# Kernel tuning notes

Measured on AMD Instinct MI355X. Metric: run time of the kernel, lower is better.

Reference implementation:

```python
import math
import jax, jax.numpy as jnp
import numpy as np

DRAGON_ITERATIONS = 12
DRAGON_SMOOTHING = 0.1


def _dragon_patterns(iterations=DRAGON_ITERATIONS, smoothing=DRAGON_SMOOTHING):
    """Deterministic (non-learned) Dragon curve patterns, matching torch impl."""
    patterns = [np.array([0.5], dtype=np.float32)]
    kernel = np.ones(3, dtype=np.float32) / 3.0
    for _ in range(1, iterations):
        prev = patterns[-1]
        n = len(prev)
        newp = np.zeros(2 * n + 1, dtype=np.float32)
        newp[:n] = prev
        newp[n] = 0.5
        newp[n + 1:] = 1.0 - prev[::-1]
        if smoothing > 0:
            # conv1d with kernel_size=3, padding=1 (zero pad) == np.convolve 'same'
            newp = np.convolve(newp, kernel, mode='same').astype(np.float32)
        newp = (newp - newp.min()) / (newp.max() - newp.min() + 1e-8)
        patterns.append(newp.astype(np.float32))
    return patterns

_PATTERNS = _dragon_patterns()


def _interp_pattern(seq_len):
    """Linearly interpolate selected dragon pattern to seq_len (static shapes)."""
    it = min(int(math.log2(seq_len)), DRAGON_ITERATIONS - 1)
    pattern = _PATTERNS[it]
    if len(pattern) == seq_len:
        w = pattern.copy()
    else:
        x_old = np.linspace(0.0, 1.0, len(pattern), dtype=np.float64)
        x_new = np.linspace(0.0, 1.0, seq_len, dtype=np.float64)
        w = np.interp(x_new, x_old, pattern.astype(np.float64)).astype(np.float32)
    return it, jnp.asarray(w)


def setup_inputs() -> dict:
    key = jax.random.key(0)
    ks = jax.random.split(key, 8)
    B, S, D = 8, 2048, 512
    query = jax.random.normal(ks[0], (B, S, D), dtype=jnp.float32)
    k = jax.random.normal(ks[1], (B, S, D), dtype=jnp.float32)
    value = jax.random.normal(ks[2], (B, S, D), dtype=jnp.float32)
    pattern_scale = jnp.ones((DRAGON_ITERATIONS,), dtype=jnp.float32)
    pattern_bias = jnp.zeros((DRAGON_ITERATIONS,), dtype=jnp.float32)
    w1 = jax.random.normal(ks[3], (DRAGON_ITERATIONS, 64), dtype=jnp.float32) * (1.0 / math.sqrt(DRAGON_ITERATIONS))
    b1 = jnp.zeros((64,), dtype=jnp.float32)
    w2 = jax.random.normal(ks[4], (64, 1), dtype=jnp.float32) * (1.0 / 8.0)
    b2 = jnp.zeros((1,), dtype=jnp.float32)
    return {"query": query, "key": k, "value": value,
            "pattern_scale": pattern_scale, "pattern_bias": pattern_bias,
            "w1": w1, "b1": b1, "w2": w2, "b2": b2}


def reference(query, key, value, pattern_scale, pattern_bias, w1, b1, w2, b2):
    B, S, D = key.shape
    it, base_w = _interp_pattern(S)
    # learned affine + softplus on dragon weights
    dragon_w = jax.nn.softplus(base_w * pattern_scale[it] + pattern_bias[it])  # [S]
    weighted_keys = key * dragon_w[None, :, None]                              # [B,S,D]
    scores = jnp.einsum('bqd,bkd->bqk', query, weighted_keys) / math.sqrt(D)   # [B,S,S]
    attn = jax.nn.softmax(scores, axis=-1)
    # blend factor from one-hot iteration features through tiny MLP
    feat = jax.nn.one_hot(it, DRAGON_ITERATIONS, dtype=query.dtype)            # [12]
    h = jax.nn.relu(feat @ w1 + b1)
    blend = jax.nn.sigmoid(h @ w2 + b2)                                        # [1]
    blend = blend[0]
    final_attn = blend * attn + (1.0 - blend) / S                              # uniform blend
    out = jnp.einsum('bqk,bkd->bqd', final_attn, value)                        # [B,S,D]
    # original does output.squeeze(1); S>1 so it's a no-op here
    return out
```

## Files before the change

### kernel.cpp

```cpp
#include <hip/hip_runtime.h>
#include <cstdint>

#define DEV __device__ __forceinline__

typedef float f32x4 __attribute__((ext_vector_type(4)));
typedef short s16x8 __attribute__((ext_vector_type(8)));

DEV unsigned short f2bf(float f){
    unsigned u = __builtin_bit_cast(unsigned, f);
    u = u + 0x7fffu + ((u >> 16) & 1u);
    return (unsigned short)(u >> 16);
}
DEV float bf2f(unsigned short h){
    unsigned u = ((unsigned)h) << 16;
    return __builtin_bit_cast(float, u);
}

typedef const void __attribute__((address_space(1)))* gcp;
typedef void __attribute__((address_space(3)))* lp;
DEV void gload_lds16(const void* g, void* l){
    __builtin_amdgcn_global_load_lds((gcp)g, (lp)l, 16, 0, 0);
}

#define SCALE_QK 0.04419417382415922f

struct Pat2 { float v[2048]; };
constexpr Pat2 make_pat2(){
    float a[4095] = {}; float b[4095] = {};
    a[0] = 0.5f; int len = 1;
    for (int it = 1; it < 12; ++it){
        int n = len, nl = 2*n + 1;
        for (int i = 0; i < nl; ++i)
            b[i] = (i < n) ? a[i] : ((i == n) ? 0.5f : 1.0f - a[2*n - i]);
        const float third = 1.0f/3.0f;
        float mn = 3.4e38f, mx = -3.4e38f;
        for (int i = 0; i < nl; ++i){
            float s = b[i]*third;
            if (i > 0)      s += b[i-1]*third;
            if (i < nl - 1) s += b[i+1]*third;
            a[i] = s;
            mn = (s < mn) ? s : mn;
            mx = (s > mx) ? s : mx;
        }
        float d = mx - mn + 1e-8f;
        for (int i = 0; i < nl; ++i) a[i] = (a[i] - mn) / d;
        len = nl;
    }
    Pat2 p{};
    for (int i = 0; i < 2048; ++i) p.v[i] = a[2*i];
    return p;
}
__device__ const Pat2 g_pat2 = make_pat2();

__global__ __launch_bounds__(256) void k_conv(
    const float* __restrict__ Q, const float* __restrict__ K,
    const float* __restrict__ V,
    unsigned short* __restrict__ Qb, unsigned short* __restrict__ Kb,
    unsigned short* __restrict__ Vt, float* __restrict__ vmean)
{
    __shared__ float sh[4480];
    int tid = threadIdx.x;
    int bx  = blockIdx.x;

    if (bx < 1024){
        const long long total4 = (long long)8*2048*512/4;
        long long stride = 1024LL*256;
        for (long long i = (long long)bx*256 + tid; i < total4; i += stride){
            long long base = i*4;
            const float4 q = *(const float4*)(Q + base);
            const float4 k = *(const float4*)(K + base);
            ushort4 qo, ko;
            qo.x = f2bf(q.x); qo.y = f2bf(q.y); qo.z = f2bf(q.z); qo.w = f2bf(q.w);
            ko.x = f2bf(k.x); ko.y = f2bf(k.y); ko.z = f2bf(k.z); ko.w = f2bf(k.w);
            *(ushort4*)(Qb + base) = qo;
            *(ushort4*)(Kb + base) = ko;
        }
        return;
    }

    int t = bx - 1024;
    int stile = t & 31, dtile = (t >> 5) & 7, b = t >> 8;
    int s0 = stile*64, d0 = dtile*64;
    float (*tile)[66] = (float(*)[66])sh;
    float* red = sh + 4224;
    int tx = tid & 63, ty = tid >> 6;
    const float* src = V + ((long long)b*2048 + s0)*512 + d0;
    #pragma unroll
    for (int r = 0; r < 16; ++r){
        int row = r*4 + ty;
        tile[row][tx] = src[(long long)row*512 + tx];
    }
    __syncthreads();
    unsigned short* dst = Vt + ((long long)b*512 + d0)*2048 + s0;
    #pragma unroll
    for (int r = 0; r < 16; ++r){
        int drow = r*4 + ty;
        dst[(long long)drow*2048 + tx] = f2bf(tile[tx][drow]);
    }
    int dcol = tid & 63, sp = tid >> 6;
    float s = 0.f;
    #pragma unroll
    for (int ii = 0; ii < 16; ++ii) s += tile[sp*16 + ii][dcol];
    red[sp*64 + dcol] = s;
    __syncthreads();
    if (sp == 0){
        float tot = red[dcol] + red[64+dcol] + red[128+dcol] + red[192+dcol];
        atomicAdd(&vmean[b*512 + d0 + dcol], tot * (1.0f/2048.0f));
    }
}

#define EPAD 140

__global__ __launch_bounds__(256) void k_gemm_qk(
    const unsigned short* __restrict__ Qb, const unsigned short* __restrict__ Kb,
    const float* __restrict__ scale, const float* __restrict__ bias,
    unsigned short* __restrict__ Sp)
{
    __shared__ unsigned short smem[128*EPAD];
    unsigned short* At = smem;
    unsigned short* Bt = smem + 8192;
    int tid = threadIdx.x;
    int lane = tid & 63, wave = tid >> 6;
    int wm = wave >> 1, wn = wave & 1;
    int ln = lane & 15, q4 = lane >> 4;
    int sx = ln & 7;
    int q0 = blockIdx.y*128, k0 = blockIdx.x*128, b = blockIdx.z;
    const unsigned short* Abase = Qb + ((long long)b*2048 + q0)*512;
    const unsigned short* Bbase = Kb + ((long long)b*2048 + k0)*512;

    f32x4 acc[4][4];
    #pragma unroll
    for (int i = 0; i < 4; ++i)
        #pragma unroll
        for (int j = 0; j < 4; ++j) acc[i][j] = (f32x4)0.0f;

    int cc = lane & 7, rg = lane >> 3;
    for (int kt = 0; kt < 8; ++kt){
        #pragma unroll
        for (int c = 0; c < 4; ++c){
            int chunk = wave*4 + c;
            int row = chunk*8 + rg;
            int gc  = cc ^ (row & 7);
            gload_lds16(Abase + (long long)row*512 + kt*64 + gc*8, &At[chunk*512]);
            gload_lds16(Bbase + (long long)row*512 + kt*64 + gc*8, &Bt[chunk*512]);
        }
        __syncthreads();
        #pragma unroll
        for (int ks = 0; ks < 2; ++ks){
            int cs = ((ks*4 + q4) ^ sx) * 8;
            s16x8 af[4], bfr[4];
            #pragma unroll
            for (int i = 0; i < 4; ++i)
                af[i] = *(const s16x8*)&At[(wm*64 + i*16 + ln)*64 + cs];
            #pragma unroll
            for (int j = 0; j < 4; ++j)
                bfr[j] = *(const s16x8*)&Bt[(wn*64 + j*16 + ln)*64 + cs];
            #pragma unroll
            for (int i = 0; i < 4; ++i)
                #pragma unroll
                for (int j = 0; j < 4; ++j)
                    acc[i][j] = __builtin_amdgcn_mfma_f32_16x16x32_bf16(af[i], bfr[j], acc[i][j], 0, 0, 0);
        }
        __syncthreads();
    }

    float sc = scale[11], bi = bias[11];
    float wq[4];
    #pragma unroll
    for (int j = 0; j < 4; ++j){
        float x = g_pat2.v[k0 + wn*64 + j*16 + ln]*sc + bi;
        wq[j] = (fmaxf(x, 0.f) + log1pf(__expf(-fabsf(x)))) * SCALE_QK;
    }
    #pragma unroll
    for (int i = 0; i < 4; ++i)
        #pragma unroll
        for (int j = 0; j < 4; ++j)
            #pragma unroll
            for (int r = 0; r < 4; ++r){
                int ql = wm*64 + i*16 + q4*4 + r;
                int kl = wn*64 + j*16 + ln;
                smem[ql*EPAD + kl] = f2bf(__expf(acc[i][j][r] * wq[j]));
            }
    __syncthreads();
    int row = tid >> 1, half = tid & 1;
    unsigned short* dstp = Sp + (long long)b*2048*2048
                              + (long long)(q0 + row)*2048 + k0 + half*64;
    const unsigned short* srcp = &smem[row*EPAD + half*64];
    #pragma unroll
    for (int u = 0; u < 8; ++u)
        *(s16x8*)(dstp + u*8) = *(const s16x8*)(srcp + u*8);
}

__global__ __launch_bounds__(256) void k_gemm_pv(
    const unsigned short* __restrict__ Sp, const unsigned short* __restrict__ Vt,
    const float* __restrict__ vmean,
    const float* __restrict__ w1, const float* __restrict__ b1,
    const float* __restrict__ w2, const float* __restrict__ b2,
    float* __restrict__ out)
{
    __shared__ unsigned short At[128*64];
    __shared__ unsigned short Bt[128*64];
    __shared__ float l_sh[128];
    __shared__ float sh_blend;
    int tid = threadIdx.x;
    int lane = tid & 63, wave = tid >> 6;
    int wm = wave >> 1, wn = wave & 1;
    int ln = lane & 15, q4 = lane >> 4;
    int sx = ln & 7;

    if (wave == 0){
        float h = fmaxf(w1[11*64 + lane] + b1[lane], 0.f);
        float c = h * w2[lane];
        #pragma unroll
        for (int off = 32; off > 0; off >>= 1) c += __shfl_xor(c, off, 64);
        if (lane == 0) sh_blend = 1.f/(1.f + __expf(-(c + b2[0])));
    }

    int g    = blockIdx.x;
    int xcd  = g & 7, slot = g >> 3;
    int pair = xcd*16 + (slot >> 2);
    int dt   = slot & 3;
    int qt   = pair & 15, b = pair >> 4;
    int q0 = qt*128, d0 = dt*128;

    const unsigned short* Abase = Sp + (long long)b*2048*2048 + (long long)q0*2048;
    const unsigned short* Bbase = Vt + ((long long)b*512 + d0)*2048;

    f32x4 acc[4][4];
    #pragma unroll
    for (int i = 0; i < 4; ++i)
        #pragma unroll
        for (int j = 0; j < 4; ++j) acc[i][j] = (f32x4)0.0f;
    float lsum[4] = {0.f, 0.f, 0.f, 0.f};

    int cc = lane & 7, rg = lane >> 3;
    for (int kt = 0; kt < 32; ++kt){
        #pragma unroll
        for (int c = 0; c < 4; ++c){
            int chunk = wave*4 + c;
            int row = chunk*8 + rg;
            int gc  = cc ^ (row & 7);
            gload_lds16(Abase + (long long)row*2048 + kt*64 + gc*8, &At[chunk*512]);
            gload_lds16(Bbase + (long long)row*2048 + kt*64 + gc*8, &Bt[chunk*512]);
        }
        __syncthreads();
        #pragma unroll
        for (int ks = 0; ks < 2; ++ks){
            int cs = ((ks*4 + q4) ^ sx) * 8;
            s16x8 af[4], bfr[4];
            #pragma unroll
            for (int i = 0; i < 4; ++i)
                af[i] = *(const s16x8*)&At[(wm*64 + i*16 + ln)*64 + cs];
            #pragma unroll
            for (int j = 0; j < 4; ++j)
                bfr[j] = *(const s16x8*)&Bt[(wn*64 + j*16 + ln)*64 + cs];
            if (wn == 0){
                #pragma unroll
                for (int i = 0; i < 4; ++i){
                    float s = 0.f;
                    #pragma unroll
                    for (int jj = 0; jj < 8; ++jj) s += bf2f((unsigned short)af[i][jj]);
                    lsum[i] += s;
                }
            }
            #pragma unroll
            for (int i = 0; i < 4; ++i)
                #pragma unroll
                for (int j = 0; j < 4; ++j)
                    acc[i][j] = __builtin_amdgcn_mfma_f32_16x16x32_bf16(af[i], bfr[j], acc[i][j], 0, 0, 0);
        }
        __syncthreads();
    }
    if (wn == 0){
        #pragma unroll
        for (int i = 0; i < 4; ++i){
            float v = lsum[i];
            v += __shfl_xor(v, 16, 64);
            v += __shfl_xor(v, 32, 64);
            if (lane < 16) l_sh[wm*64 + i*16 + lane] = v;
        }
    }
    __syncthreads();

    float blend = sh_blend;
    float ib = 1.0f - blend;
    float* obase = out + ((long long)b*2048 + q0)*512 + d0;
    float vm[4];
    #pragma unroll
    for (int j = 0; j < 4; ++j) vm[j] = vmean[b*512 + d0 + wn*64 + j*16 + ln];
    #pragma unroll
    for (int i = 0; i < 4; ++i){
        #pragma unroll
        for (int r = 0; r < 4; ++r){
            int ql = wm*64 + i*16 + q4*4 + r;
            float linv = 1.0f / l_sh[ql];
            #pragma unroll
            for (int j = 0; j < 4; ++j){
                int dl = wn*64 + j*16 + ln;
                obase[(long long)ql*512 + dl] = blend*acc[i][j][r]*linv + ib*vm[j];
            }
        }
    }
}

extern "C" void kernel_launch(void* const* d_in, const int* in_sizes, int n_in,
                              void* d_out, int out_size, void* d_ws, size_t ws_size,
                              hipStream_t stream)
{
    (void)in_sizes; (void)n_in; (void)out_size; (void)ws_size;
    const float* Q  = (const float*)d_in[0];
    const float* K  = (const float*)d_in[1];
    const float* V  = (const float*)d_in[2];
    const float* ps = (const float*)d_in[3];
    const float* pb = (const float*)d_in[4];
    const float* w1 = (const float*)d_in[5];
    const float* b1 = (const float*)d_in[6];
    const float* w2 = (const float*)d_in[7];
    const float* b2 = (const float*)d_in[8];
    float* out = (float*)d_out;

    char* ws = (char*)d_ws;
    float* vmean           = (float*)(ws);
    size_t off = 32768;
    unsigned short* Qb     = (unsigned short*)(ws + off);
    unsigned short* Kb     = (unsigned short*)(ws + off + (size_t)16*1024*1024);
    unsigned short* Vt     = (unsigned short*)(ws + off + (size_t)32*1024*1024);
    unsigned short* Sp     = (unsigned short*)(ws + off + (size_t)48*1024*1024);

    hipMemsetAsync(vmean, 0, 4096*sizeof(float), stream);
    hipLaunchKernelGGL(k_conv,    dim3(3072),      dim3(256), 0, stream,
                       Q, K, V, Qb, Kb, Vt, vmean);
    hipLaunchKernelGGL(k_gemm_qk, dim3(16, 16, 8), dim3(256), 0, stream,
                       Qb, Kb, ps, pb, Sp);
    hipLaunchKernelGGL(k_gemm_pv, dim3(512),       dim3(256), 0, stream,
                       Sp, Vt, vmean, w1, b1, w2, b2, out);
}
```

Measured before the change: 266.2 us.

## Compute V column means inside PV GEMM and drop QK epilogue LDS staging

The V column mean is no longer built in the conversion kernel with shared-memory reductions and atomics. It is now computed in the PV GEMM by summing the bf16 V tiles already loaded into LDS, which removes the memset launch and the atomic traffic. The QK GEMM epilogue now writes scores straight from registers to global memory as 2-byte stores instead of staging them through padded LDS for 16-byte vector stores. The conversion kernel also gets twice as many blocks for the Q/K cast. The risks are less coalesced score writes and extra VALU work in the PV inner loop, and the mean is now taken from bf16-rounded values.

Result: faster. 259.4 us (-2.6%).

```diff
diff --git a/kernel.cpp b/kernel.cpp
--- a/kernel.cpp
+++ b/kernel.cpp
@@ -56,15 +56,15 @@
     const float* __restrict__ Q, const float* __restrict__ K,
     const float* __restrict__ V,
     unsigned short* __restrict__ Qb, unsigned short* __restrict__ Kb,
-    unsigned short* __restrict__ Vt, float* __restrict__ vmean)
+    unsigned short* __restrict__ Vt)
 {
-    __shared__ float sh[4480];
+    __shared__ float sh[4224];
     int tid = threadIdx.x;
     int bx  = blockIdx.x;
 
-    if (bx < 1024){
+    if (bx < 2048){
         const long long total4 = (long long)8*2048*512/4;
-        long long stride = 1024LL*256;
+        long long stride = 2048LL*256;
         for (long long i = (long long)bx*256 + tid; i < total4; i += stride){
             long long base = i*4;
             const float4 q = *(const float4*)(Q + base);
@@ -78,11 +78,10 @@
         return;
     }
 
-    int t = bx - 1024;
+    int t = bx - 2048;
     int stile = t & 31, dtile = (t >> 5) & 7, b = t >> 8;
     int s0 = stile*64, d0 = dtile*64;
     float (*tile)[66] = (float(*)[66])sh;
-    float* red = sh + 4224;
     int tx = tid & 63, ty = tid >> 6;
     const float* src = V + ((long long)b*2048 + s0)*512 + d0;
     #pragma unroll
@@ -97,28 +96,15 @@
         int drow = r*4 + ty;
         dst[(long long)drow*2048 + tx] = f2bf(tile[tx][drow]);
     }
-    int dcol = tid & 63, sp = tid >> 6;
-    float s = 0.f;
-    #pragma unroll
-    for (int ii = 0; ii < 16; ++ii) s += tile[sp*16 + ii][dcol];
-    red[sp*64 + dcol] = s;
-    __syncthreads();
-    if (sp == 0){
-        float tot = red[dcol] + red[64+dcol] + red[128+dcol] + red[192+dcol];
-        atomicAdd(&vmean[b*512 + d0 + dcol], tot * (1.0f/2048.0f));
-    }
-}
-
-#define EPAD 140
+}
 
 __global__ __launch_bounds__(256) void k_gemm_qk(
     const unsigned short* __restrict__ Qb, const unsigned short* __restrict__ Kb,
     const float* __restrict__ scale, const float* __restrict__ bias,
     unsigned short* __restrict__ Sp)
 {
-    __shared__ unsigned short smem[128*EPAD];
-    unsigned short* At = smem;
-    unsigned short* Bt = smem + 8192;
+    __shared__ unsigned short At[128*64];
+    __shared__ unsigned short Bt[128*64];
     int tid = threadIdx.x;
     int lane = tid & 63, wave = tid >> 6;
     int wm = wave >> 1, wn = wave & 1;
@@ -171,29 +157,23 @@
         float x = g_pat2.v[k0 + wn*64 + j*16 + ln]*sc + bi;
         wq[j] = (fmaxf(x, 0.f) + log1pf(__expf(-fabsf(x)))) * SCALE_QK;
     }
-    #pragma unroll
-    for (int i = 0; i < 4; ++i)
-        #pragma unroll
-        for (int j = 0; j < 4; ++j)
+    unsigned short* outp = Sp + (long long)b*2048*2048;
+    #pragma unroll
+    for (int i = 0; i < 4; ++i){
+        #pragma unroll
+        for (int j = 0; j < 4; ++j){
             #pragma unroll
             for (int r = 0; r < 4; ++r){
-                int ql = wm*64 + i*16 + q4*4 + r;
-                int kl = wn*64 + j*16 + ln;
-                smem[ql*EPAD + kl] = f2bf(__expf(acc[i][j][r] * wq[j]));
+                int q = q0 + wm*64 + i*16 + q4*4 + r;
+                int k = k0 + wn*64 + j*16 + ln;
+                outp[(long long)q*2048 + k] = f2bf(__expf(acc[i][j][r] * wq[j]));
             }
-    __syncthreads();
-    int row = tid >> 1, half = tid & 1;
-    unsigned short* dstp = Sp + (long long)b*2048*2048
-                              + (long long)(q0 + row)*2048 + k0 + half*64;
-    const unsigned short* srcp = &smem[row*EPAD + half*64];
-    #pragma unroll
-    for (int u = 0; u < 8; ++u)
-        *(s16x8*)(dstp + u*8) = *(const s16x8*)(srcp + u*8);
+        }
+    }
 }
 
 __global__ __launch_bounds__(256) void k_gemm_pv(
     const unsigned short* __restrict__ Sp, const unsigned short* __restrict__ Vt,
-    const float* __restrict__ vmean,
     const float* __restrict__ w1, const float* __restrict__ b1,
     const float* __restrict__ w2, const float* __restrict__ b2,
     float* __restrict__ out)
@@ -201,6 +181,7 @@
     __shared__ unsigned short At[128*64];
     __shared__ unsigned short Bt[128*64];
     __shared__ float l_sh[128];
+    __shared__ float v_sh[128];
     __shared__ float sh_blend;
     int tid = threadIdx.x;
     int lane = tid & 63, wave = tid >> 6;
@@ -232,6 +213,7 @@
         #pragma unroll
         for (int j = 0; j < 4; ++j) acc[i][j] = (f32x4)0.0f;
     float lsum[4] = {0.f, 0.f, 0.f, 0.f};
+    float vsum[4] = {0.f, 0.f, 0.f, 0.f};
 
     int cc = lane & 7, rg = lane >> 3;
     for (int kt = 0; kt < 32; ++kt){
@@ -264,6 +246,13 @@
                 }
             }
             #pragma unroll
+            for (int j = 0; j < 4; ++j){
+                float s = 0.f;
+                #pragma unroll
+                for (int jj = 0; jj < 8; ++jj) s += bf2f((unsigned short)bfr[j][jj]);
+                vsum[j] += s;
+            }
+            #pragma unroll
             for (int i = 0; i < 4; ++i)
                 #pragma unroll
                 for (int j = 0; j < 4; ++j)
@@ -280,6 +269,13 @@
             if (lane < 16) l_sh[wm*64 + i*16 + lane] = v;
         }
     }
+    #pragma unroll
+    for (int j = 0; j < 4; ++j){
+        float v = vsum[j];
+        v += __shfl_xor(v, 16, 64);
+        v += __shfl_xor(v, 32, 64);
+        if (wm == 0 && lane < 16) v_sh[wn*64 + j*16 + lane] = v * (1.0f/2048.0f);
+    }
     __syncthreads();
 
     float blend = sh_blend;
@@ -287,7 +283,7 @@
     float* obase = out + ((long long)b*2048 + q0)*512 + d0;
     float vm[4];
     #pragma unroll
-    for (int j = 0; j < 4; ++j) vm[j] = vmean[b*512 + d0 + wn*64 + j*16 + ln];
+    for (int j = 0; j < 4; ++j) vm[j] = v_sh[wn*64 + j*16 + ln];
     #pragma unroll
     for (int i = 0; i < 4; ++i){
         #pragma unroll
@@ -320,18 +316,15 @@
     float* out = (float*)d_out;
 
     char* ws = (char*)d_ws;
-    float* vmean           = (float*)(ws);
-    size_t off = 32768;
-    unsigned short* Qb     = (unsigned short*)(ws + off);
-    unsigned short* Kb     = (unsigned short*)(ws + off + (size_t)16*1024*1024);
-    unsigned short* Vt     = (unsigned short*)(ws + off + (size_t)32*1024*1024);
-    unsigned short* Sp     = (unsigned short*)(ws + off + (size_t)48*1024*1024);
-
-    hipMemsetAsync(vmean, 0, 4096*sizeof(float), stream);
-    hipLaunchKernelGGL(k_conv,    dim3(3072),      dim3(256), 0, stream,
-                       Q, K, V, Qb, Kb, Vt, vmean);
+    unsigned short* Qb     = (unsigned short*)(ws);
+    unsigned short* Kb     = (unsigned short*)(ws + (size_t)16*1024*1024);
+    unsigned short* Vt     = (unsigned short*)(ws + (size_t)32*1024*1024);
+    unsigned short* Sp     = (unsigned short*)(ws + (size_t)48*1024*1024);
+
+    hipLaunchKernelGGL(k_conv,    dim3(4096),      dim3(256), 0, stream,
+                       Q, K, V, Qb, Kb, Vt);
     hipLaunchKernelGGL(k_gemm_qk, dim3(16, 16, 8), dim3(256), 0, stream,
                        Qb, Kb, ps, pb, Sp);
     hipLaunchKernelGGL(k_gemm_pv, dim3(512),       dim3(256), 0, stream,
-                       Sp, Vt, vmean, w1, b1, w2, b2, out);
-}
+                       Sp, Vt, w1, b1, w2, b2, out);
+}
```
